# Kernel tuning notes

Hardware: AMD Instinct MI355X
Metric: run time of the kernel (lower is better)

Reference implementation:

```python
import jax, jax.numpy as jnp
import numpy as np

N_KERNELS = 16
KSIZE = 3
B, H, W = 16, 512, 512

def setup_inputs() -> dict:
    key = jax.random.key(0)
    k1, k2, k3, k4 = jax.random.split(key, 4)
    x = jax.random.uniform(k1, (B, 1, H, W), dtype=jnp.float32)
    kernels = jax.random.normal(k2, (N_KERNELS, 1, KSIZE, KSIZE), dtype=jnp.float32)
    reactants = jax.random.normal(k3, (N_KERNELS,), dtype=jnp.float32)
    products = jax.random.normal(k4, (N_KERNELS,), dtype=jnp.float32)
    return {"x": x, "kernels": kernels, "reactants": reactants, "products": products}

def reference(x, kernels, reactants, products):
    # All n_kernels 1->1 convs batched as a single 1->n_kernels conv.
    pad = KSIZE // 2
    N = jax.lax.conv_general_dilated(
        x, kernels,
        window_strides=(1, 1),
        padding=[(pad, pad), (pad, pad)],
        dimension_numbers=("NCHW", "OIHW", "NCHW"),
    )  # [B, n_kernels, H, W]
    GAIN = 10.0
    condition = jax.nn.sigmoid(GAIN * (N - reactants[None, :, None, None]))
    # x has 1 channel; broadcasts against the n_kernels axis
    update = condition * (products[None, :, None, None] - x)
    delta = jnp.sum(update, axis=1, keepdims=True)  # sum over kernels -> [B,1,H,W]
    return jnp.clip(x + delta, 0.0, 1.0)
```

## Files before the change

### kernel.cpp

```cpp
#include <hip/hip_runtime.h>


#define NK 16
#define BATCH 16
#define H 512
#define W 512
#define G2 14.4269504088896340f

typedef float f2 __attribute__((ext_vector_type(2)));

#if __has_builtin(__builtin_amdgcn_exp2f)
#define EXP2F(x) __builtin_amdgcn_exp2f(x)
#else
#define EXP2F(x) exp2f(x)
#endif

#if __has_builtin(__builtin_elementwise_fma)
#define FMA2(a, b, c) __builtin_elementwise_fma((a), (b), (c))
#else
#define FMA2(a, b, c) ((a) * (b) + (c))
#endif

static __device__ __forceinline__ f2 bc2(float s) { f2 r; r.x = s; r.y = s; return r; }

typedef const __attribute__((address_space(4))) float cfloat;

__global__ __launch_bounds__(256, 4) void nca_kernel(
    const float* __restrict__ x,
    const float* __restrict__ kernels,
    const float* __restrict__ reactants,
    const float* __restrict__ products,
    float* __restrict__ out)
{
    const int idx = blockIdx.x * blockDim.x + threadIdx.x;
    const int w4 = (idx & 127) << 2;
    const int h0 = ((idx >> 7) & 255) << 1;
    const int b  = idx >> 15;

    const float* xb = x + (size_t)b * (H * W);

    float v[4][6];
#pragma unroll
    for (int r = 0; r < 4; ++r) {
        const int row = h0 + r - 1;
        if (row >= 0 && row < H) {
            const float* xr = xb + row * W;
            const float4 c = *(const float4*)(xr + w4);
            v[r][1] = c.x; v[r][2] = c.y; v[r][3] = c.z; v[r][4] = c.w;
            v[r][0] = (w4 > 0)     ? xr[w4 - 1] : 0.0f;
            v[r][5] = (w4 + 4 < W) ? xr[w4 + 4] : 0.0f;
        } else {
#pragma unroll
            for (int c = 0; c < 6; ++c) v[r][c] = 0.0f;
        }
    }

    f2 sl[4][5];
#pragma unroll
    for (int r = 0; r < 4; ++r)
#pragma unroll
        for (int s = 0; s < 5; ++s) { sl[r][s].x = v[r][s]; sl[r][s].y = v[r][s + 1]; }

    cfloat* kc = (cfloat*)kernels;
    cfloat* rc = (cfloat*)reactants;
    cfloat* pc = (cfloat*)products;

    f2 s0[2][2], s1[2][2];
#pragma unroll
    for (int py = 0; py < 2; ++py)
#pragma unroll
        for (int g = 0; g < 2; ++g) { s0[py][g] = bc2(0.0f); s1[py][g] = bc2(0.0f); }

    const f2 mg2 = bc2(-G2);
    const f2 one = bc2(1.0f);

#pragma unroll
    for (int k = 0; k < NK; ++k) {
        f2 wk[9];
#pragma unroll
        for (int i = 0; i < 9; ++i) wk[i] = bc2(kc[k * 9 + i]);
        const f2 c2 = bc2(G2 * rc[k]);
        const f2 pk = bc2(pc[k]);

#pragma unroll
        for (int py = 0; py < 2; ++py) {
#pragma unroll
            for (int g = 0; g < 2; ++g) {
                f2 n = bc2(0.0f);
#pragma unroll
                for (int r = 0; r < 3; ++r)
#pragma unroll
                    for (int c = 0; c < 3; ++c)
                        n = FMA2(sl[py + r][2 * g + c], wk[r * 3 + c], n);
                const f2 z = FMA2(mg2, n, c2);
                f2 e;
                e.x = EXP2F(z.x);
                e.y = EXP2F(z.y);
                const f2 d = e + one;
                f2 sig;
                sig.x = __builtin_amdgcn_rcpf(d.x);
                sig.y = __builtin_amdgcn_rcpf(d.y);
                s0[py][g] = s0[py][g] + sig;
                s1[py][g] = FMA2(sig, pk, s1[py][g]);
            }
        }
    }

#pragma unroll
    for (int py = 0; py < 2; ++py) {
        float4 o;
#pragma unroll
        for (int g = 0; g < 2; ++g) {
            const f2 xv = sl[py + 1][2 * g + 1];
            f2 res = FMA2(-xv, s0[py][g], xv + s1[py][g]);
            res.x = fminf(fmaxf(res.x, 0.0f), 1.0f);
            res.y = fminf(fmaxf(res.y, 0.0f), 1.0f);
            if (g == 0) { o.x = res.x; o.y = res.y; }
            else        { o.z = res.x; o.w = res.y; }
        }
        *(float4*)(out + ((size_t)(b * H + h0 + py) * W + w4)) = o;
    }
}

extern "C" void kernel_launch(void* const* d_in, const int* in_sizes, int n_in,
                              void* d_out, int out_size, void* d_ws, size_t ws_size,
                              hipStream_t stream) {
    const float* x         = (const float*)d_in[0];
    const float* kernels   = (const float*)d_in[1];
    const float* reactants = (const float*)d_in[2];
    const float* products  = (const float*)d_in[3];
    float* out = (float*)d_out;

    const int total_tiles = BATCH * (H / 2) * (W / 4);
    nca_kernel<<<total_tiles / 256, 256, 0, stream>>>(x, kernels, reactants, products, out);
}
```

Baseline: 91.00 us.

## Batch sigmoid reciprocals into one rcp per four pixels and shrink tile to 1x4

Each thread now handles one row of four pixels instead of a 2x4 tile. The four sigmoid denominators share a single hardware reciprocal through product tricks, and the exponent input is clamped at 28 so the product cannot overflow. Occupancy is raised to 6 waves per EU, and the output address is computed directly from the thread index. The costs are more redundant row loads and several extra multiplies per group, which trade transcendental throughput for VALU work. The clamp adds a slight precision change.

```diff
diff --git a/kernel.cpp b/kernel.cpp
--- a/kernel.cpp
+++ b/kernel.cpp
@@ -21,11 +21,19 @@
 #define FMA2(a, b, c) ((a) * (b) + (c))
 #endif
 
+#if __has_builtin(__builtin_elementwise_min)
+#define MIN2(a, b) __builtin_elementwise_min((a), (b))
+#else
+static __device__ __forceinline__ f2 MIN2(f2 a, f2 b) {
+    f2 r; r.x = fminf(a.x, b.x); r.y = fminf(a.y, b.y); return r;
+}
+#endif
+
 static __device__ __forceinline__ f2 bc2(float s) { f2 r; r.x = s; r.y = s; return r; }
 
 typedef const __attribute__((address_space(4))) float cfloat;
 
-__global__ __launch_bounds__(256, 4) void nca_kernel(
+__global__ __launch_bounds__(256, 6) void nca_kernel(
     const float* __restrict__ x,
     const float* __restrict__ kernels,
     const float* __restrict__ reactants,
@@ -34,15 +42,15 @@
 {
     const int idx = blockIdx.x * blockDim.x + threadIdx.x;
     const int w4 = (idx & 127) << 2;
-    const int h0 = ((idx >> 7) & 255) << 1;
-    const int b  = idx >> 15;
+    const int h  = (idx >> 7) & 511;
+    const int b  = idx >> 16;
 
     const float* xb = x + (size_t)b * (H * W);
 
-    float v[4][6];
+    float v[3][6];
 #pragma unroll
-    for (int r = 0; r < 4; ++r) {
-        const int row = h0 + r - 1;
+    for (int r = 0; r < 3; ++r) {
+        const int row = h + r - 1;
         if (row >= 0 && row < H) {
             const float* xr = xb + row * W;
             const float4 c = *(const float4*)(xr + w4);
@@ -55,9 +63,9 @@
         }
     }
 
-    f2 sl[4][5];
+    f2 sl[3][5];
 #pragma unroll
-    for (int r = 0; r < 4; ++r)
+    for (int r = 0; r < 3; ++r)
 #pragma unroll
         for (int s = 0; s < 5; ++s) { sl[r][s].x = v[r][s]; sl[r][s].y = v[r][s + 1]; }
 
@@ -65,14 +73,12 @@
     cfloat* rc = (cfloat*)reactants;
     cfloat* pc = (cfloat*)products;
 
-    f2 s0[2][2], s1[2][2];
-#pragma unroll
-    for (int py = 0; py < 2; ++py)
-#pragma unroll
-        for (int g = 0; g < 2; ++g) { s0[py][g] = bc2(0.0f); s1[py][g] = bc2(0.0f); }
+    f2 s0[2], s1[2];
+    s0[0] = bc2(0.0f); s0[1] = bc2(0.0f);
+    s1[0] = bc2(0.0f); s1[1] = bc2(0.0f);
 
-    const f2 mg2 = bc2(-G2);
-    const f2 one = bc2(1.0f);
+    const f2 mg2  = bc2(-G2);
+    const f2 zcap = bc2(28.0f);
 
 #pragma unroll
     for (int k = 0; k < NK; ++k) {
@@ -82,44 +88,51 @@
         const f2 c2 = bc2(G2 * rc[k]);
         const f2 pk = bc2(pc[k]);
 
+        f2 d[2];
 #pragma unroll
-        for (int py = 0; py < 2; ++py) {
+        for (int g = 0; g < 2; ++g) {
+            f2 n = bc2(0.0f);
 #pragma unroll
-            for (int g = 0; g < 2; ++g) {
-                f2 n = bc2(0.0f);
+            for (int r = 0; r < 3; ++r)
 #pragma unroll
-                for (int r = 0; r < 3; ++r)
-#pragma unroll
-                    for (int c = 0; c < 3; ++c)
-                        n = FMA2(sl[py + r][2 * g + c], wk[r * 3 + c], n);
-                const f2 z = FMA2(mg2, n, c2);
-                f2 e;
-                e.x = EXP2F(z.x);
-                e.y = EXP2F(z.y);
-                const f2 d = e + one;
-                f2 sig;
-                sig.x = __builtin_amdgcn_rcpf(d.x);
-                sig.y = __builtin_amdgcn_rcpf(d.y);
-                s0[py][g] = s0[py][g] + sig;
-                s1[py][g] = FMA2(sig, pk, s1[py][g]);
-            }
+                for (int c = 0; c < 3; ++c)
+                    n = FMA2(sl[r][2 * g + c], wk[r * 3 + c], n);
+            f2 z = FMA2(mg2, n, c2);
+            z = MIN2(z, zcap);
+            f2 e;
+            e.x = EXP2F(z.x);
+            e.y = EXP2F(z.y);
+            d[g] = e + bc2(1.0f);
         }
+
+        const float t1 = d[0].x * d[0].y;
+        const float t2 = d[1].x * d[1].y;
+        const float r4 = __builtin_amdgcn_rcpf(t1 * t2);
+        const float r01 = r4 * t2;
+        const float r23 = r4 * t1;
+        f2 sig0, sig1;
+        sig0.x = r01 * d[0].y;
+        sig0.y = r01 * d[0].x;
+        sig1.x = r23 * d[1].y;
+        sig1.y = r23 * d[1].x;
+
+        s0[0] = s0[0] + sig0;
+        s0[1] = s0[1] + sig1;
+        s1[0] = FMA2(sig0, pk, s1[0]);
+        s1[1] = FMA2(sig1, pk, s1[1]);
     }
 
+    float4 o;
 #pragma unroll
-    for (int py = 0; py < 2; ++py) {
-        float4 o;
-#pragma unroll
-        for (int g = 0; g < 2; ++g) {
-            const f2 xv = sl[py + 1][2 * g + 1];
-            f2 res = FMA2(-xv, s0[py][g], xv + s1[py][g]);
-            res.x = fminf(fmaxf(res.x, 0.0f), 1.0f);
-            res.y = fminf(fmaxf(res.y, 0.0f), 1.0f);
-            if (g == 0) { o.x = res.x; o.y = res.y; }
-            else        { o.z = res.x; o.w = res.y; }
-        }
-        *(float4*)(out + ((size_t)(b * H + h0 + py) * W + w4)) = o;
+    for (int g = 0; g < 2; ++g) {
+        const f2 xv = sl[1][2 * g + 1];
+        f2 res = FMA2(-xv, s0[g], xv + s1[g]);
+        res.x = fminf(fmaxf(res.x, 0.0f), 1.0f);
+        res.y = fminf(fmaxf(res.y, 0.0f), 1.0f);
+        if (g == 0) { o.x = res.x; o.y = res.y; }
+        else        { o.z = res.x; o.w = res.y; }
     }
+    *(float4*)(out + (size_t)idx * 4) = o;
 }
 
 extern "C" void kernel_launch(void* const* d_in, const int* in_sizes, int n_in,
@@ -131,6 +144,6 @@
     const float* products  = (const float*)d_in[3];
     float* out = (float*)d_out;
 
-    const int total_tiles = BATCH * (H / 2) * (W / 4);
-    nca_kernel<<<total_tiles / 256, 256, 0, stream>>>(x, kernels, reactants, products, out);
+    const int total_strips = BATCH * H * (W / 4);
+    nca_kernel<<<total_strips / 256, 256, 0, stream>>>(x, kernels, reactants, products, out);
 }
```

New measurement: 95.10 us. 1.05x slower.
